# Performance work log

Hardware: AMD Instinct MI355X
Metric: run time of the kernel (lower is better)

The kernel has to match this reference:

```python
import jax, jax.numpy as jnp
import numpy as np

N_NODES = 50000
N_EDGES = 800000
IN_FEAT = 64
HID = 128
NUM_CLASSES = 32


def _glorot(key, shape):
    fan_in, fan_out = shape[0], shape[1]
    lim = jnp.sqrt(6.0 / (fan_in + fan_out))
    return jax.random.uniform(key, shape, jnp.float32, -lim, lim)


def setup_inputs() -> dict:
    key = jax.random.key(0)
    ks = jax.random.split(key, 8)
    x = jax.random.normal(ks[0], (N_NODES, IN_FEAT), dtype=jnp.float32)
    edge_index = jax.random.randint(ks[1], (2, N_EDGES), 0, N_NODES, dtype=jnp.int64 if jax.config.jax_enable_x64 else jnp.int32)
    W1 = _glorot(ks[2], (IN_FEAT, HID))
    b1 = jnp.zeros((HID,), jnp.float32)
    W2 = _glorot(ks[3], (HID, NUM_CLASSES))
    b2 = jnp.zeros((NUM_CLASSES,), jnp.float32)
    Wc = _glorot(ks[4], (NUM_CLASSES, NUM_CLASSES))
    bc = jnp.zeros((NUM_CLASSES,), jnp.float32)
    return {"x": x, "edge_index": edge_index, "W1": W1, "b1": b1,
            "W2": W2, "b2": b2, "Wc": Wc, "bc": bc}


def _gcn_conv(x, src, dst, norm, W, b):
    # x' = scatter_add(norm * gather(xW, src), dst) + b   (PyG GCNConv, self-loops included in src/dst)
    h = x @ W                                   # [N, out]
    msg = h[src] * norm[:, None]                # [E+N, out] gather + scale
    out = jax.ops.segment_sum(msg, dst, num_segments=N_NODES)  # scatter-add
    return out + b


def reference(x, edge_index, W1, b1, W2, b2, Wc, bc):
    # add self-loops (PyG GCNConv default add_self_loops=True)
    loops = jnp.arange(N_NODES, dtype=edge_index.dtype)
    src = jnp.concatenate([edge_index[0], loops])
    dst = jnp.concatenate([edge_index[1], loops])
    # symmetric normalization: deg over targets of A + I
    deg = jax.ops.segment_sum(jnp.ones_like(src, dtype=x.dtype), dst, num_segments=N_NODES)
    dinv = jnp.where(deg > 0, jax.lax.rsqrt(deg), 0.0)
    norm = dinv[src] * dinv[dst]                # [E+N]

    h = _gcn_conv(x, src, dst, norm, W1, b1)
    h = jax.nn.relu(h)                          # dropout p=0.0 -> identity
    h = _gcn_conv(h, src, dst, norm, W2, b2)
    out = h @ Wc + bc
    return (out, h)
```

## Files before the change

### kernel.cpp

```cpp
#include <hip/hip_runtime.h>


static constexpr int N  = 50000;
static constexpr int E  = 800000;
static constexpr int F0 = 64;
static constexpr int F1 = 128;
static constexpr int F2 = 32;

static constexpr int BSH    = 7;
static constexpr int BNODES = 128;
static constexpr int BMASK  = 127;
static constexpr int NBUK   = 392;
static constexpr int NSEG   = 4;
static constexpr int SEGCAP = 768;
static constexpr int BCAP   = NSEG * SEGCAP;
static constexpr int CHUNK  = 4096;
static constexpr int NCHUNK = 196;

typedef __attribute__((ext_vector_type(8))) short short8v;
typedef __attribute__((ext_vector_type(4))) float float4v;

__device__ __forceinline__ unsigned int f2bf(float f) {
  unsigned int u = __float_as_uint(f);
  return (u + 0x7fffu + ((u >> 16) & 1u)) >> 16;
}
__device__ __forceinline__ float bflo(unsigned int u) {
  return __uint_as_float(u << 16);
}
__device__ __forceinline__ float bfhi(unsigned int u) {
  return __uint_as_float(u & 0xffff0000u);
}

__global__ __launch_bounds__(512) void k_bucket(const int* __restrict__ src,
    const int* __restrict__ dst, int* __restrict__ gcur,
    unsigned int* __restrict__ ebuf) {
  __shared__ int hl[NBUK];
  int t = threadIdx.x, c = blockIdx.x;
  const int sub = c & (NSEG - 1);
  for (int i = t; i < NBUK; i += 512) hl[i] = 0;
  __syncthreads();
  int e0 = c * CHUNK, m = min(CHUNK, E - e0);
  int dreg[8];
  if (m == CHUNK) {
    const int4* dv4 = reinterpret_cast<const int4*>(dst + e0);
    int4 a = dv4[t * 2], b = dv4[t * 2 + 1];
    dreg[0] = a.x; dreg[1] = a.y; dreg[2] = a.z; dreg[3] = a.w;
    dreg[4] = b.x; dreg[5] = b.y; dreg[6] = b.z; dreg[7] = b.w;
    #pragma unroll
    for (int k = 0; k < 8; ++k) atomicAdd(&hl[dreg[k] >> BSH], 1);
  } else {
    #pragma unroll
    for (int k = 0; k < 8; ++k) {
      int i = t * 8 + k;
      dreg[k] = (i < m) ? dst[e0 + i] : -1;
      if (i < m) atomicAdd(&hl[dreg[k] >> BSH], 1);
    }
  }
  __syncthreads();
  for (int i = t; i < NBUK; i += 512) {
    int cc = hl[i];
    int rbase = (cc > 0) ? atomicAdd(&gcur[(i * NSEG + sub) * 16], cc) : 0;
    hl[i] = i * BCAP + sub * SEGCAP + rbase;
  }
  __syncthreads();
  if (m == CHUNK) {
    const int4* sv4 = reinterpret_cast<const int4*>(src + e0);
    int4 a = sv4[t * 2], b = sv4[t * 2 + 1];
    int sreg[8] = {a.x, a.y, a.z, a.w, b.x, b.y, b.z, b.w};
    #pragma unroll
    for (int k = 0; k < 8; ++k) {
      int d = dreg[k];
      int pos = atomicAdd(&hl[d >> BSH], 1);
      ebuf[pos] = (unsigned int)sreg[k] | ((unsigned int)(d & BMASK) << 16);
    }
  } else {
    #pragma unroll
    for (int k = 0; k < 8; ++k) {
      int i = t * 8 + k;
      if (i < m) {
        int d = dreg[k], s = src[e0 + i];
        int pos = atomicAdd(&hl[d >> BSH], 1);
        ebuf[pos] = (unsigned int)s | ((unsigned int)(d & BMASK) << 16);
      }
    }
  }
}

__global__ __launch_bounds__(512) void k_csr(const unsigned int* __restrict__ ebuf,
    const int* __restrict__ gcur, const float* __restrict__ x,
    int* __restrict__ cnt, int* __restrict__ rowend, float* __restrict__ dinv,
    int* __restrict__ ssrc, unsigned short* __restrict__ xs16) {
  __shared__ int cl[BNODES], sc[BNODES], cur[BNODES];
  __shared__ float dl[BNODES];
  int t = threadIdx.x, b = blockIdx.x;
  int base = b * BCAP;
  int node0 = b << BSH;
  int ms[NSEG];
  #pragma unroll
  for (int s = 0; s < NSEG; ++s) ms[s] = gcur[(b * NSEG + s) * 16];
  if (t < BNODES) cl[t] = 0;
  __syncthreads();
  unsigned int ereg[NSEG * 2];
  #pragma unroll
  for (int s = 0; s < NSEG; ++s) {
    int msz = ms[s], sb = base + s * SEGCAP;
    #pragma unroll
    for (int k = 0; k < 2; ++k) {
      int i = t + k * 512;
      unsigned int p = 0xFFFFFFFFu;
      if (i < msz) {
        p = ebuf[sb + i];
        atomicAdd(&cl[(p >> 16) & BMASK], 1);
      }
      ereg[s * 2 + k] = p;
    }
  }
  __syncthreads();
  int v = 0;
  if (t < BNODES) { v = cl[t]; sc[t] = v; }
  __syncthreads();
  for (int off = 1; off < BNODES; off <<= 1) {
    int u = (t >= off && t < BNODES) ? sc[t - off] : 0;
    __syncthreads();
    if (t < BNODES) sc[t] += u;
    __syncthreads();
  }
  if (t < BNODES) {
    int excl = sc[t] - v;
    cur[t] = excl;
    float dv = rsqrtf((float)(v + 1));
    dl[t] = dv;
    int g = node0 + t;
    if (g < N) {
      cnt[g]    = v;
      rowend[g] = base + excl + v;
      dinv[g]   = dv;
    }
  }
  __syncthreads();
  #pragma unroll
  for (int s = 0; s < NSEG; ++s) {
    #pragma unroll
    for (int k = 0; k < 2; ++k) {
      unsigned int p = ereg[s * 2 + k];
      if (p != 0xFFFFFFFFu) {
        int d = (p >> 16) & BMASK;
        int r = atomicAdd(&cur[d], 1);
        ssrc[base + r] = (int)(p & 0xFFFFu);
      }
    }
  }
  for (int i = t; i < BNODES * (F0 / 8); i += 512) {
    int nl = i >> 3, oc = i & 7;
    int n = node0 + nl;
    if (n < N) {
      float4 a  = reinterpret_cast<const float4*>(x)[n * 16 + oc * 2];
      float4 bb = reinterpret_cast<const float4*>(x)[n * 16 + oc * 2 + 1];
      float d = dl[nl];
      uint4 pk;
      pk.x = f2bf(a.x * d)  | (f2bf(a.y * d) << 16);
      pk.y = f2bf(a.z * d)  | (f2bf(a.w * d) << 16);
      pk.z = f2bf(bb.x * d) | (f2bf(bb.y * d) << 16);
      pk.w = f2bf(bb.z * d) | (f2bf(bb.w * d) << 16);
      reinterpret_cast<uint4*>(xs16)[(size_t)n * 8 + oc] = pk;
    }
  }
}

__global__ __launch_bounds__(256) void k_agg1(const int* __restrict__ rowend,
    const int* __restrict__ cnt, const int* __restrict__ ssrc,
    const unsigned short* __restrict__ xs16, const float* __restrict__ dinv,
    unsigned short* __restrict__ AX16) {
  int gw = (blockIdx.x * 256 + threadIdx.x) >> 6;
  int lane = threadIdx.x & 63;
  if (gw >= N) return;
  int end   = __builtin_amdgcn_readfirstlane(rowend[gw]);
  int deg   = __builtin_amdgcn_readfirstlane(cnt[gw]);
  int start = end - deg;
  const int g = lane >> 3, fl = lane & 7;
  const uint4* xsv = reinterpret_cast<const uint4*>(xs16);
  float acc[8];
  #pragma unroll
  for (int k = 0; k < 8; ++k) acc[k] = 0.f;
  for (int e0 = start; e0 < end; e0 += 32) {
    if (e0 + 32 <= end) {
      int s0 = ssrc[e0 + g];
      int s1 = ssrc[e0 + 8 + g];
      int s2 = ssrc[e0 + 16 + g];
      int s3 = ssrc[e0 + 24 + g];
      uint4 u0 = xsv[(size_t)s0 * 8 + fl];
      uint4 u1 = xsv[(size_t)s1 * 8 + fl];
      uint4 u2 = xsv[(size_t)s2 * 8 + fl];
      uint4 u3 = xsv[(size_t)s3 * 8 + fl];
      acc[0] += bflo(u0.x); acc[1] += bfhi(u0.x);
      acc[2] += bflo(u0.y); acc[3] += bfhi(u0.y);
      acc[4] += bflo(u0.z); acc[5] += bfhi(u0.z);
      acc[6] += bflo(u0.w); acc[7] += bfhi(u0.w);
      acc[0] += bflo(u1.x); acc[1] += bfhi(u1.x);
      acc[2] += bflo(u1.y); acc[3] += bfhi(u1.y);
      acc[4] += bflo(u1.z); acc[5] += bfhi(u1.z);
      acc[6] += bflo(u1.w); acc[7] += bfhi(u1.w);
      acc[0] += bflo(u2.x); acc[1] += bfhi(u2.x);
      acc[2] += bflo(u2.y); acc[3] += bfhi(u2.y);
      acc[4] += bflo(u2.z); acc[5] += bfhi(u2.z);
      acc[6] += bflo(u2.w); acc[7] += bfhi(u2.w);
      acc[0] += bflo(u3.x); acc[1] += bfhi(u3.x);
      acc[2] += bflo(u3.y); acc[3] += bfhi(u3.y);
      acc[4] += bflo(u3.z); acc[5] += bfhi(u3.z);
      acc[6] += bflo(u3.w); acc[7] += bfhi(u3.w);
    } else {
      #pragma unroll
      for (int q = 0; q < 4; ++q) {
        int j = e0 + 8 * q + g;
        int s = ssrc[(j < end) ? j : start];
        float mm = (j < end) ? 1.f : 0.f;
        uint4 u = xsv[(size_t)s * 8 + fl];
        acc[0] = fmaf(bflo(u.x), mm, acc[0]); acc[1] = fmaf(bfhi(u.x), mm, acc[1]);
        acc[2] = fmaf(bflo(u.y), mm, acc[2]); acc[3] = fmaf(bfhi(u.y), mm, acc[3]);
        acc[4] = fmaf(bflo(u.z), mm, acc[4]); acc[5] = fmaf(bfhi(u.z), mm, acc[5]);
        acc[6] = fmaf(bflo(u.w), mm, acc[6]); acc[7] = fmaf(bfhi(u.w), mm, acc[7]);
      }
    }
  }
  #pragma unroll
  for (int r = 8; r < 64; r <<= 1) {
    #pragma unroll
    for (int k = 0; k < 8; ++k) acc[k] += __shfl_xor(acc[k], r);
  }
  if (lane < 8) {
    uint4 su = xsv[(size_t)gw * 8 + fl];
    float dv = dinv[gw];
    float o[8];
    o[0] = (acc[0] + bflo(su.x)) * dv; o[1] = (acc[1] + bfhi(su.x)) * dv;
    o[2] = (acc[2] + bflo(su.y)) * dv; o[3] = (acc[3] + bfhi(su.y)) * dv;
    o[4] = (acc[4] + bflo(su.z)) * dv; o[5] = (acc[5] + bfhi(su.z)) * dv;
    o[6] = (acc[6] + bflo(su.w)) * dv; o[7] = (acc[7] + bfhi(su.w)) * dv;
    uint4 pk;
    pk.x = f2bf(o[0]) | (f2bf(o[1]) << 16);
    pk.y = f2bf(o[2]) | (f2bf(o[3]) << 16);
    pk.z = f2bf(o[4]) | (f2bf(o[5]) << 16);
    pk.w = f2bf(o[6]) | (f2bf(o[7]) << 16);
    reinterpret_cast<uint4*>(AX16)[(size_t)gw * 8 + fl] = pk;
  }
}

__global__ __launch_bounds__(256) void k_gemm12(const unsigned short* __restrict__ AX16,
    const float* __restrict__ W1, const float* __restrict__ b1,
    const float* __restrict__ W2, const float* __restrict__ dinv,
    unsigned short* __restrict__ H2s16) {
  __shared__ float arena[6656];
  unsigned int* Wfu = reinterpret_cast<unsigned int*>(arena);
  const short8v* Wf8 = reinterpret_cast<const short8v*>(arena);
  unsigned short* H1b = reinterpret_cast<unsigned short*>(arena);
  unsigned int* Wf2u = reinterpret_cast<unsigned int*>(arena + 4608);
  const short8v* Wf2_8 = reinterpret_cast<const short8v*>(arena + 4608);
  const short8v* H1b8 = reinterpret_cast<const short8v*>(arena);
  const int tid = threadIdx.x;
  const int row0 = blockIdx.x * 64;
  for (int i = tid; i < 4096; i += 256) {
    int jh = i & 3, l = (i >> 2) & 63, f = i >> 8;
    int k0  = (f & 1) * 32 + ((l >> 4) << 3) + jh * 2;
    int col = (f >> 1) * 16 + (l & 15);
    float w0 = W1[k0 * F1 + col];
    float w1 = W1[(k0 + 1) * F1 + col];
    Wfu[i] = f2bf(w0) | (f2bf(w1) << 16);
  }
  __syncthreads();
  const int w = tid >> 6, l = tid & 63;
  const int nrow = row0 + w * 16 + (l & 15);
  const short8v* axv8 = reinterpret_cast<const short8v*>(AX16);
  short8v A0 = axv8[(size_t)nrow * 8 + (l >> 4)];
  short8v A1 = axv8[(size_t)nrow * 8 + 4 + (l >> 4)];
  float4v acc[8];
  #pragma unroll
  for (int ct = 0; ct < 8; ++ct)
    #pragma unroll
    for (int r = 0; r < 4; ++r) acc[ct][r] = 0.f;
  #pragma unroll
  for (int ct = 0; ct < 8; ++ct) {
    short8v B0 = Wf8[(ct * 2 + 0) * 64 + l];
    short8v B1 = Wf8[(ct * 2 + 1) * 64 + l];
    acc[ct] = __builtin_amdgcn_mfma_f32_16x16x32_bf16(A0, B0, acc[ct], 0, 0, 0);
    acc[ct] = __builtin_amdgcn_mfma_f32_16x16x32_bf16(A1, B1, acc[ct], 0, 0, 0);
  }
  __syncthreads();
  #pragma unroll
  for (int ct = 0; ct < 8; ++ct) {
    int col = ct * 16 + (l & 15);
    float bb = b1[col];
    #pragma unroll
    for (int r = 0; r < 4; ++r) {
      int row = w * 16 + ((l >> 4) << 2) + r;
      H1b[row * 136 + col] = (unsigned short)f2bf(fmaxf(acc[ct][r] + bb, 0.f));
    }
  }
  for (int i = tid; i < 2048; i += 256) {
    int jh = i & 3, ll = (i >> 2) & 63, f = i >> 8;
    int ks = f & 3, ctB = f >> 2;
    int k0  = ks * 32 + ((ll >> 4) << 3) + jh * 2;
    int col = ctB * 16 + (ll & 15);
    float w0 = W2[k0 * F2 + col];
    float w1 = W2[(k0 + 1) * F2 + col];
    Wf2u[i] = f2bf(w0) | (f2bf(w1) << 16);
  }
  __syncthreads();
  float4v acc2[2];
  #pragma unroll
  for (int i = 0; i < 2; ++i)
    #pragma unroll
    for (int r = 0; r < 4; ++r) acc2[i][r] = 0.f;
  #pragma unroll
  for (int ks = 0; ks < 4; ++ks) {
    short8v Af = H1b8[(w * 16 + (l & 15)) * 17 + ks * 4 + (l >> 4)];
    acc2[0] = __builtin_amdgcn_mfma_f32_16x16x32_bf16(Af, Wf2_8[(0 * 4 + ks) * 64 + l], acc2[0], 0, 0, 0);
    acc2[1] = __builtin_amdgcn_mfma_f32_16x16x32_bf16(Af, Wf2_8[(1 * 4 + ks) * 64 + l], acc2[1], 0, 0, 0);
  }
  #pragma unroll
  for (int r = 0; r < 4; ++r) {
    int n = row0 + w * 16 + ((l >> 4) << 2) + r;
    if (n < N) {
      float d = dinv[n];
      H2s16[(size_t)n * F2 + (l & 15)]      = (unsigned short)f2bf(acc2[0][r] * d);
      H2s16[(size_t)n * F2 + 16 + (l & 15)] = (unsigned short)f2bf(acc2[1][r] * d);
    }
  }
}

__global__ __launch_bounds__(256) void k_agg2h(const int* __restrict__ rowend,
    const int* __restrict__ cnt, const int* __restrict__ ssrc,
    const unsigned short* __restrict__ H2s16, const float* __restrict__ dinv,
    const float* __restrict__ b2, const float* __restrict__ Wc,
    const float* __restrict__ bc, float* __restrict__ h2,
    float* __restrict__ out) {
  __shared__ float Wcs[F2][F2];
  __shared__ float h2row[4][F2];
  const int tid = threadIdx.x;
  for (int i = tid; i < F2 * F2; i += 256) Wcs[i >> 5][i & 31] = Wc[i];
  __syncthreads();
  int gw = (blockIdx.x * 256 + tid) >> 6;
  int lane = tid & 63;
  int w = tid >> 6;
  if (gw >= N) return;
  int end   = __builtin_amdgcn_readfirstlane(rowend[gw]);
  int deg   = __builtin_amdgcn_readfirstlane(cnt[gw]);
  int start = end - deg;
  const int g = lane >> 2, fl = lane & 3;
  const uint4* hv = reinterpret_cast<const uint4*>(H2s16);
  float acc[8];
  #pragma unroll
  for (int k = 0; k < 8; ++k) acc[k] = 0.f;
  for (int e0 = start; e0 < end; e0 += 32) {
    if (e0 + 32 <= end) {
      int s0 = ssrc[e0 + g];
      int s1 = ssrc[e0 + 16 + g];
      uint4 u0 = hv[(size_t)s0 * 4 + fl];
      uint4 u1 = hv[(size_t)s1 * 4 + fl];
      acc[0] += bflo(u0.x); acc[1] += bfhi(u0.x);
      acc[2] += bflo(u0.y); acc[3] += bfhi(u0.y);
      acc[4] += bflo(u0.z); acc[5] += bfhi(u0.z);
      acc[6] += bflo(u0.w); acc[7] += bfhi(u0.w);
      acc[0] += bflo(u1.x); acc[1] += bfhi(u1.x);
      acc[2] += bflo(u1.y); acc[3] += bfhi(u1.y);
      acc[4] += bflo(u1.z); acc[5] += bfhi(u1.z);
      acc[6] += bflo(u1.w); acc[7] += bfhi(u1.w);
    } else {
      #pragma unroll
      for (int q = 0; q < 2; ++q) {
        int j = e0 + 16 * q + g;
        int s = ssrc[(j < end) ? j : start];
        float mm = (j < end) ? 1.f : 0.f;
        uint4 u = hv[(size_t)s * 4 + fl];
        acc[0] = fmaf(bflo(u.x), mm, acc[0]); acc[1] = fmaf(bfhi(u.x), mm, acc[1]);
        acc[2] = fmaf(bflo(u.y), mm, acc[2]); acc[3] = fmaf(bfhi(u.y), mm, acc[3]);
        acc[4] = fmaf(bflo(u.z), mm, acc[4]); acc[5] = fmaf(bfhi(u.z), mm, acc[5]);
        acc[6] = fmaf(bflo(u.w), mm, acc[6]); acc[7] = fmaf(bfhi(u.w), mm, acc[7]);
      }
    }
  }
  #pragma unroll
  for (int r = 4; r < 64; r <<= 1) {
    #pragma unroll
    for (int k = 0; k < 8; ++k) acc[k] += __shfl_xor(acc[k], r);
  }
  float dv = dinv[gw];
  if (lane < 4) {
    uint4 su = hv[(size_t)gw * 4 + fl];
    float o[8];
    o[0] = dv * (acc[0] + bflo(su.x)) + b2[fl * 8 + 0];
    o[1] = dv * (acc[1] + bfhi(su.x)) + b2[fl * 8 + 1];
    o[2] = dv * (acc[2] + bflo(su.y)) + b2[fl * 8 + 2];
    o[3] = dv * (acc[3] + bfhi(su.y)) + b2[fl * 8 + 3];
    o[4] = dv * (acc[4] + bflo(su.z)) + b2[fl * 8 + 4];
    o[5] = dv * (acc[5] + bfhi(su.z)) + b2[fl * 8 + 5];
    o[6] = dv * (acc[6] + bflo(su.w)) + b2[fl * 8 + 6];
    o[7] = dv * (acc[7] + bfhi(su.w)) + b2[fl * 8 + 7];
    *reinterpret_cast<float4*>(&h2[(size_t)gw * F2 + fl * 8])     = *reinterpret_cast<float4*>(o);
    *reinterpret_cast<float4*>(&h2[(size_t)gw * F2 + fl * 8 + 4]) = *reinterpret_cast<float4*>(o + 4);
    #pragma unroll
    for (int k = 0; k < 8; ++k) h2row[w][fl * 8 + k] = o[k];
  }
  int f = lane & 31, half = lane >> 5;
  float acco = 0.f;
  #pragma unroll
  for (int kk = 0; kk < 16; ++kk) {
    int k = kk + 16 * half;
    acco = fmaf(h2row[w][k], Wcs[k][f], acco);
  }
  acco += __shfl_xor(acco, 32);
  if (half == 0) out[(size_t)gw * F2 + f] = acco + bc[f];
}

extern "C" void kernel_launch(void* const* d_in, const int* in_sizes, int n_in,
                              void* d_out, int out_size, void* d_ws, size_t ws_size,
                              hipStream_t stream) {
  const float* x  = (const float*)d_in[0];
  const int*   ei = (const int*)d_in[1];
  const int*   src = ei;
  const int*   dst = ei + E;
  const float* W1 = (const float*)d_in[2];
  const float* b1 = (const float*)d_in[3];
  const float* W2 = (const float*)d_in[4];
  const float* b2 = (const float*)d_in[5];
  const float* Wc = (const float*)d_in[6];
  const float* bc = (const float*)d_in[7];

  float* out = (float*)d_out;
  float* h2  = out + (size_t)N * F2;

  int*   cnt     = (int*)d_ws;
  int*   rowend  = cnt + N;
  int*   gcur    = rowend + N;
  float* dinv    = (float*)(gcur + NBUK * NSEG * 16);
  int*   ssrc    = (int*)(dinv + N);
  unsigned int* ebuf = (unsigned int*)(ssrc + NBUK * BCAP);
  unsigned short* xs16 = (unsigned short*)(ebuf + NBUK * BCAP);
  unsigned short* AX16 = xs16 + (size_t)N * F0;
  unsigned short* H2s16 = AX16 + (size_t)N * F0;

  hipMemsetAsync(gcur, 0, NBUK * NSEG * 16 * sizeof(int), stream);
  k_bucket<<<NCHUNK, 512, 0, stream>>>(src, dst, gcur, ebuf);
  k_csr   <<<NBUK,   512, 0, stream>>>(ebuf, gcur, x, cnt, rowend, dinv, ssrc, xs16);

  k_agg1  <<<(N + 3) / 4, 256, 0, stream>>>(rowend, cnt, ssrc, xs16, dinv, AX16);
  k_gemm12<<<(N + 63) / 64, 256, 0, stream>>>(AX16, W1, b1, W2, dinv, H2s16);
  k_agg2h <<<(N + 3) / 4, 256, 0, stream>>>(rowend, cnt, ssrc, H2s16, dinv, b2, Wc, bc, h2, out);
}
```

Baseline: 97.82 us.

## Replace global atomic bucket counters with per-chunk fixed slots and histogram prefix scan

The bucketing kernel stops taking global atomic offsets into segmented bucket regions. Each (bucket, chunk) pair now gets a fixed slot of CCAP entries, and per-chunk counts go to a histogram. The CSR kernel prefix-scans that histogram and gathers the slots into shared memory before counting and scattering. This removes the memset and the global atomics. In exchange it adds a 512-wide scan with many syncs, serial per-thread copy loops, and an overflow risk if any chunk puts more than 44 edges into one bucket (the expected count is about 10, so this is unlikely but unguarded).

Result: faster. 93.00 us (-4.9%).

```diff
diff --git a/kernel.cpp b/kernel.cpp
--- a/kernel.cpp
+++ b/kernel.cpp
@@ -11,11 +11,10 @@
 static constexpr int BNODES = 128;
 static constexpr int BMASK  = 127;
 static constexpr int NBUK   = 392;
-static constexpr int NSEG   = 4;
-static constexpr int SEGCAP = 768;
-static constexpr int BCAP   = NSEG * SEGCAP;
 static constexpr int CHUNK  = 4096;
 static constexpr int NCHUNK = 196;
+static constexpr int CCAP   = 44;
+static constexpr int BCAP   = 3072;
 
 typedef __attribute__((ext_vector_type(8))) short short8v;
 typedef __attribute__((ext_vector_type(4))) float float4v;
@@ -32,11 +31,10 @@
 }
 
 __global__ __launch_bounds__(512) void k_bucket(const int* __restrict__ src,
-    const int* __restrict__ dst, int* __restrict__ gcur,
+    const int* __restrict__ dst, int* __restrict__ hist,
     unsigned int* __restrict__ ebuf) {
   __shared__ int hl[NBUK];
   int t = threadIdx.x, c = blockIdx.x;
-  const int sub = c & (NSEG - 1);
   for (int i = t; i < NBUK; i += 512) hl[i] = 0;
   __syncthreads();
   int e0 = c * CHUNK, m = min(CHUNK, E - e0);
@@ -58,9 +56,8 @@
   }
   __syncthreads();
   for (int i = t; i < NBUK; i += 512) {
-    int cc = hl[i];
-    int rbase = (cc > 0) ? atomicAdd(&gcur[(i * NSEG + sub) * 16], cc) : 0;
-    hl[i] = i * BCAP + sub * SEGCAP + rbase;
+    hist[i * NCHUNK + c] = hl[i];
+    hl[i] = (i * NCHUNK + c) * CCAP;
   }
   __syncthreads();
   if (m == CHUNK) {
@@ -87,34 +84,32 @@
 }
 
 __global__ __launch_bounds__(512) void k_csr(const unsigned int* __restrict__ ebuf,
-    const int* __restrict__ gcur, const float* __restrict__ x,
+    const int* __restrict__ hist, const float* __restrict__ x,
     int* __restrict__ cnt, int* __restrict__ rowend, float* __restrict__ dinv,
     int* __restrict__ ssrc, unsigned short* __restrict__ xs16) {
+  __shared__ int s512[512];
+  __shared__ unsigned int eb[BCAP];
   __shared__ int cl[BNODES], sc[BNODES], cur[BNODES];
   __shared__ float dl[BNODES];
   int t = threadIdx.x, b = blockIdx.x;
   int base = b * BCAP;
   int node0 = b << BSH;
-  int ms[NSEG];
-  #pragma unroll
-  for (int s = 0; s < NSEG; ++s) ms[s] = gcur[(b * NSEG + s) * 16];
+  int cntc = (t < NCHUNK) ? hist[b * NCHUNK + t] : 0;
+  s512[t] = cntc; __syncthreads();
+  for (int off = 1; off < 512; off <<= 1) {
+    int u = (t >= off) ? s512[t - off] : 0;
+    __syncthreads(); s512[t] += u; __syncthreads();
+  }
+  int pref = s512[t] - cntc;
+  int m = s512[511];
   if (t < BNODES) cl[t] = 0;
-  __syncthreads();
-  unsigned int ereg[NSEG * 2];
-  #pragma unroll
-  for (int s = 0; s < NSEG; ++s) {
-    int msz = ms[s], sb = base + s * SEGCAP;
-    #pragma unroll
-    for (int k = 0; k < 2; ++k) {
-      int i = t + k * 512;
-      unsigned int p = 0xFFFFFFFFu;
-      if (i < msz) {
-        p = ebuf[sb + i];
-        atomicAdd(&cl[(p >> 16) & BMASK], 1);
-      }
-      ereg[s * 2 + k] = p;
-    }
-  }
+  if (t < NCHUNK && cntc > 0) {
+    const unsigned int* rp = ebuf + ((size_t)b * NCHUNK + t) * CCAP;
+    for (int i = 0; i < cntc; ++i) eb[pref + i] = rp[i];
+  }
+  __syncthreads();
+  for (int i = t; i < m; i += 512)
+    atomicAdd(&cl[(eb[i] >> 16) & BMASK], 1);
   __syncthreads();
   int v = 0;
   if (t < BNODES) { v = cl[t]; sc[t] = v; }
@@ -138,17 +133,11 @@
     }
   }
   __syncthreads();
-  #pragma unroll
-  for (int s = 0; s < NSEG; ++s) {
-    #pragma unroll
-    for (int k = 0; k < 2; ++k) {
-      unsigned int p = ereg[s * 2 + k];
-      if (p != 0xFFFFFFFFu) {
-        int d = (p >> 16) & BMASK;
-        int r = atomicAdd(&cur[d], 1);
-        ssrc[base + r] = (int)(p & 0xFFFFu);
-      }
-    }
+  for (int i = t; i < m; i += 512) {
+    unsigned int p = eb[i];
+    int d = (p >> 16) & BMASK;
+    int r = atomicAdd(&cur[d], 1);
+    ssrc[base + r] = (int)(p & 0xFFFFu);
   }
   for (int i = t; i < BNODES * (F0 / 8); i += 512) {
     int nl = i >> 3, oc = i & 7;
@@ -429,17 +418,16 @@
 
   int*   cnt     = (int*)d_ws;
   int*   rowend  = cnt + N;
-  int*   gcur    = rowend + N;
-  float* dinv    = (float*)(gcur + NBUK * NSEG * 16);
+  int*   hist    = rowend + N;
+  float* dinv    = (float*)(hist + NBUK * NCHUNK);
   int*   ssrc    = (int*)(dinv + N);
   unsigned int* ebuf = (unsigned int*)(ssrc + NBUK * BCAP);
-  unsigned short* xs16 = (unsigned short*)(ebuf + NBUK * BCAP);
+  unsigned short* xs16 = (unsigned short*)(ebuf + (size_t)NBUK * NCHUNK * CCAP);
   unsigned short* AX16 = xs16 + (size_t)N * F0;
   unsigned short* H2s16 = AX16 + (size_t)N * F0;
 
-  hipMemsetAsync(gcur, 0, NBUK * NSEG * 16 * sizeof(int), stream);
-  k_bucket<<<NCHUNK, 512, 0, stream>>>(src, dst, gcur, ebuf);
-  k_csr   <<<NBUK,   512, 0, stream>>>(ebuf, gcur, x, cnt, rowend, dinv, ssrc, xs16);
+  k_bucket<<<NCHUNK, 512, 0, stream>>>(src, dst, hist, ebuf);
+  k_csr   <<<NBUK,   512, 0, stream>>>(ebuf, hist, x, cnt, rowend, dinv, ssrc, xs16);
 
   k_agg1  <<<(N + 3) / 4, 256, 0, stream>>>(rowend, cnt, ssrc, xs16, dinv, AX16);
   k_gemm12<<<(N + 63) / 64, 256, 0, stream>>>(AX16, W1, b1, W2, dinv, H2s16);
```
